# Optimization experiments

Measured on AMD Instinct MI355X. Metric: run time of the kernel, lower is better.

The kernel has to match this reference:

```python
import jax, jax.numpy as jnp
import numpy as np

N = 16384      # batch size
F = 1024       # n_features
H = 256        # n_dim (latent)


def setup_inputs() -> dict:
    key = jax.random.key(0)
    ks = jax.random.split(key, 6)
    X = jax.random.normal(ks[0], (N, F), dtype=jnp.float32)
    We = jax.random.normal(ks[1], (F, H), dtype=jnp.float32) / np.sqrt(F).astype(np.float32)
    be = jnp.zeros((H,), dtype=jnp.float32)
    Wd = jax.random.normal(ks[2], (H, F), dtype=jnp.float32) / np.sqrt(H).astype(np.float32)
    bd = jnp.zeros((F,), dtype=jnp.float32)
    Wc = jax.random.normal(ks[3], (H, 1), dtype=jnp.float32) / np.sqrt(H).astype(np.float32)
    bc = jnp.zeros((1,), dtype=jnp.float32)
    s = jax.random.randint(ks[4], (N,), 0, 2, dtype=jnp.int32)  # protected attribute labels in {0,1}
    return {"X": X, "We": We, "be": be, "Wd": Wd, "bd": bd, "Wc": Wc, "bc": bc, "s": s, "p": 1}


def reference(X, We, be, Wd, bd, Wc, bc, s, p):
    # encoder / decoder (single Linear each, as in the default NRL construction)
    g = X @ We + be                      # [N, H]
    rec = g @ Wd + bd                    # [N, F]
    mse_mean = jnp.mean((rec - X) ** 2)  # MSELoss is built with reduction='sum' but forward uses torch.mean(pow(...)) directly

    # critic scores for ALL rows (critics share weights: [module]*n_protected)
    c = (g @ Wc + bc)[:, 0]              # [N]

    # masked pairwise L1: sum_{i in P, j notin P} |c_i - c_j|
    mp = (s == p)                        # rows where s == p
    mpf = mp.astype(c.dtype)
    mrf = (~mp).astype(c.dtype)
    Dmat = jnp.abs(c[:, None] - c[None, :])   # [N, N] pairwise L1 (cdist equivalent)
    total = mpf @ (Dmat @ mrf)                # mp^T D mr == cdist(c_p, c_rest, p=1).sum()

    w_dist_count = mp.sum()                   # == w_dist.shape[0] (number of protected rows)
    w_dist_mean = total / w_dist_count.astype(c.dtype)

    return (mse_mean, jnp.asarray(rec.shape[0]), w_dist_mean, w_dist_count)
```

## Files before the change

### kernel.cpp

```cpp
#include <hip/hip_runtime.h>
#include <hip/hip_bf16.h>
#include <cstdint>

#define NR 16384
#define NF 1024
#define NH 256

typedef __bf16 bf16x8 __attribute__((ext_vector_type(8)));
typedef float f32x4 __attribute__((ext_vector_type(4)));
typedef unsigned short us8 __attribute__((ext_vector_type(8)));

static __device__ __forceinline__ unsigned short f2bf(float f) {
    unsigned u = __float_as_uint(f);
    u += 0x7FFFu + ((u >> 16) & 1u);
    return (unsigned short)(u >> 16);
}
static __device__ __forceinline__ float bf2f(unsigned short h) {
    return __uint_as_float(((unsigned)h) << 16);
}


__global__ __launch_bounds__(256) void prep_kernel(
    const float* __restrict__ X, const float* __restrict__ We,
    const float* __restrict__ Wd,
    unsigned short* __restrict__ Xpk, unsigned short* __restrict__ Wepk,
    unsigned short* __restrict__ Wdpk, float* __restrict__ hdr) {
    const int b = blockIdx.x, t = threadIdx.x;
    if (b == 0 && t < 192) hdr[t] = 0.f;
    if (b < 1024) {
        __shared__ float tile[16 * 272];
        const int r0 = b * 16;
#pragma unroll
        for (int ch = 0; ch < 4; ++ch) {
            const int c0 = ch * 256;
#pragma unroll
            for (int p = 0; p < 4; ++p) {
                int idx = t + 256 * p;
                int r = idx >> 6, c4 = idx & 63;
                *(float4*)&tile[r * 272 + c4 * 4] =
                    *(const float4*)(X + (size_t)(r0 + r) * NF + c0 + c4 * 4);
            }
            __syncthreads();
#pragma unroll
            for (int p = 0; p < 2; ++p) {
                int u = t + 256 * p;
                int cell = u >> 6, lane = u & 63;
                int m = lane & 15, q = lane >> 4;
                const float* src = &tile[m * 272 + cell * 32 + q * 8];
                us8 v;
#pragma unroll
                for (int e = 0; e < 8; e++) v[e] = f2bf(src[e]);
                *(us8*)&Xpk[((size_t)(b * 32 + ch * 8 + cell)) * 512 + lane * 8] = v;
            }
            __syncthreads();
        }
    } else if (b < 1040) {
        const int nb = b - 1024;
        const int lane = t & 63, q = lane >> 4, li = lane & 15, idx = t >> 6;
#pragma unroll
        for (int p = 0; p < 8; p++) {
            const int kc = idx + 4 * p;
            us8 v;
#pragma unroll
            for (int e = 0; e < 8; e++)
                v[e] = f2bf(We[(size_t)(kc * 32 + q * 8 + e) * NH + nb * 16 + li]);
            *(us8*)&Wepk[((size_t)(nb * 32 + kc)) * 512 + lane * 8] = v;
        }
    } else {
        const int nb4 = b - 1040;
        const int lane = t & 63, q = lane >> 4, li = lane & 15, idx = t >> 6;
#pragma unroll
        for (int p = 0; p < 8; p++) {
            const int c = nb4 * 32 + idx + 4 * p;
            const int nb = c >> 3, kc = c & 7;
            us8 v;
#pragma unroll
            for (int e = 0; e < 8; e++)
                v[e] = f2bf(Wd[(size_t)(kc * 32 + q * 8 + e) * NF + nb * 16 + li]);
            *(us8*)&Wdpk[((size_t)(nb * 8 + kc)) * 512 + lane * 8] = v;
        }
    }
}

__global__ __launch_bounds__(256) void fused_kernel(
    const unsigned short* __restrict__ Xpk,
    const unsigned short* __restrict__ Wepk, const unsigned short* __restrict__ Wdpk,
    const float* __restrict__ be, const float* __restrict__ bd,
    const float* __restrict__ Wc,
    float* __restrict__ cpart, float* __restrict__ hdr) {
    __shared__ unsigned short gs[32 * 256];
    __shared__ float credu[4][32];
    __shared__ float msred[4];
    const int t = threadIdx.x;
    const int b = blockIdx.x, m0 = b * 32;
    const int w = t >> 6, lane = t & 63, q = lane >> 4, li = lane & 15;
    const int wn = w * 64;

    const unsigned short* Ap0 = Xpk + ((size_t)(b * 2) * 32) * 512 + lane * 8;
    const unsigned short* Ap1 = Ap0 + (size_t)32 * 512;
    const unsigned short* Bp[4];
#pragma unroll
    for (int j = 0; j < 4; j++)
        Bp[j] = Wepk + ((size_t)(w * 4 + j) * 32) * 512 + lane * 8;

    us8 fa[2][2], fb[2][4];
#pragma unroll
    for (int z = 0; z < 2; ++z) {
        fa[z][0] = *(const us8*)(Ap0 + z * 512);
        fa[z][1] = *(const us8*)(Ap1 + z * 512);
#pragma unroll
        for (int j = 0; j < 4; j++) fb[z][j] = *(const us8*)(Bp[j] + z * 512);
    }
    f32x4 acc[2][4] = {};
#pragma unroll
    for (int kc = 0; kc < 32; ++kc) {
        const int cb = kc & 1;
        us8 na0, na1, nbv[4];
        const bool pf = (kc + 2 < 32);
        if (pf) {
            na0 = *(const us8*)(Ap0 + (kc + 2) * 512);
            na1 = *(const us8*)(Ap1 + (kc + 2) * 512);
#pragma unroll
            for (int j = 0; j < 4; j++) nbv[j] = *(const us8*)(Bp[j] + (kc + 2) * 512);
        }
        bf16x8 a0 = __builtin_bit_cast(bf16x8, fa[cb][0]);
        bf16x8 a1 = __builtin_bit_cast(bf16x8, fa[cb][1]);
#pragma unroll
        for (int j = 0; j < 4; j++) {
            bf16x8 bf = __builtin_bit_cast(bf16x8, fb[cb][j]);
            acc[0][j] = __builtin_amdgcn_mfma_f32_16x16x32_bf16(bf, a0, acc[0][j], 0, 0, 0);
            acc[1][j] = __builtin_amdgcn_mfma_f32_16x16x32_bf16(bf, a1, acc[1][j], 0, 0, 0);
        }
        if (pf) {
            fa[cb][0] = na0; fa[cb][1] = na1;
#pragma unroll
            for (int j = 0; j < 4; j++) fb[cb][j] = nbv[j];
        }
    }

#pragma unroll
    for (int i = 0; i < 2; i++) {
        float csum = 0.f;
        const int ml = i * 16 + li;
#pragma unroll
        for (int j = 0; j < 4; j++) {
            const int colb = wn + j * 16 + q * 4;
            float4 be4 = *(const float4*)&be[colb];
            float4 wc4 = *(const float4*)&Wc[colb];
            float v0 = acc[i][j][0] + be4.x;
            float v1 = acc[i][j][1] + be4.y;
            float v2 = acc[i][j][2] + be4.z;
            float v3 = acc[i][j][3] + be4.w;
            csum += v0 * wc4.x + v1 * wc4.y + v2 * wc4.z + v3 * wc4.w;
            ushort4 st = { f2bf(v0), f2bf(v1), f2bf(v2), f2bf(v3) };
            const int phys = ((colb >> 3)) ^ ml;
            *(ushort4*)&gs[ml * 256 + phys * 8 + (q & 1) * 4] = st;
        }
        csum += __shfl_down(csum, 32);
        csum += __shfl_down(csum, 16);
        if (lane < 16) credu[w][i * 16 + lane] = csum;
    }
    __syncthreads();
    if (t < 32)
        cpart[m0 + t] = credu[0][t] + credu[1][t] + credu[2][t] + credu[3][t];

    const unsigned short* Wp = Wdpk + lane * 8;
    us8 gb[2][4];
#pragma unroll
    for (int z = 0; z < 2; ++z)
#pragma unroll
        for (int j = 0; j < 4; j++)
            gb[z][j] = *(const us8*)(Wp + ((size_t)((w * 4 + j) * 8 + z)) * 512);

    float lsum = 0.f;
    f32x4 a2[2][4] = {};
#pragma unroll
    for (int it = 0; it < 32; ++it) {
        const int cb = it & 1, pass = it >> 3, kc = it & 7;
        us8 nbv[4];
        const bool pf = (it + 2 < 32);
        if (pf) {
            const int p2 = (it + 2) >> 3, k2 = (it + 2) & 7;
#pragma unroll
            for (int j = 0; j < 4; j++)
                nbv[j] = *(const us8*)(Wp + ((size_t)((p2 * 16 + w * 4 + j) * 8 + k2)) * 512);
        }
        bf16x8 af[2];
#pragma unroll
        for (int i = 0; i < 2; i++) {
            const int ml = i * 16 + li;
            const int phys = (kc * 4 + q) ^ ml;
            af[i] = __builtin_bit_cast(bf16x8, *(const us8*)&gs[ml * 256 + phys * 8]);
        }
#pragma unroll
        for (int j = 0; j < 4; j++) {
            bf16x8 bf = __builtin_bit_cast(bf16x8, gb[cb][j]);
            a2[0][j] = __builtin_amdgcn_mfma_f32_16x16x32_bf16(bf, af[0], a2[0][j], 0, 0, 0);
            a2[1][j] = __builtin_amdgcn_mfma_f32_16x16x32_bf16(bf, af[1], a2[1][j], 0, 0, 0);
        }
        if (pf) {
#pragma unroll
            for (int j = 0; j < 4; j++) gb[cb][j] = nbv[j];
        }
        if (kc == 7) {
#pragma unroll
            for (int i = 0; i < 2; i++) {
                const int mbp = b * 2 + i;
#pragma unroll
                for (int j = 0; j < 4; j++) {
                    const int colb = pass * 256 + wn + j * 16 + q * 4;
                    float4 bd4 = *(const float4*)&bd[colb];
                    const int kcx = pass * 8 + w * 2 + (j >> 1);
                    const int qp = (j & 1) * 2 + (q >> 1), h = q & 1;
                    ushort4 xv = *(const ushort4*)&Xpk[((size_t)(mbp * 32 + kcx)) * 512 +
                                                       (qp * 16 + li) * 8 + h * 4];
                    float d0 = a2[i][j][0] + bd4.x - bf2f(xv.x);
                    float d1 = a2[i][j][1] + bd4.y - bf2f(xv.y);
                    float d2 = a2[i][j][2] + bd4.z - bf2f(xv.z);
                    float d3 = a2[i][j][3] + bd4.w - bf2f(xv.w);
                    lsum += d0 * d0 + d1 * d1 + d2 * d2 + d3 * d3;
                    a2[i][j] = (f32x4){0.f, 0.f, 0.f, 0.f};
                }
            }
        }
    }
#pragma unroll
    for (int o = 32; o; o >>= 1) lsum += __shfl_down(lsum, o);
    if (lane == 0) msred[w] = lsum;
    __syncthreads();
    if (t == 0)
        atomicAdd(&hdr[b & 63], msred[0] + msred[1] + msred[2] + msred[3]);
}

__global__ __launch_bounds__(256) void compact_kernel(
    const float* __restrict__ c, const int* __restrict__ s, const int* __restrict__ pv,
    float* __restrict__ cP, float* __restrict__ cR, int* __restrict__ cnt) {
    int i = blockIdx.x * 256 + threadIdx.x;
    float ci = c[i];
    bool pr = (s[i] == pv[0]);
    int lane = threadIdx.x & 63;
    unsigned long long m = __ballot(pr);
    {
        int cm = __popcll(m);
        int base = 0;
        if (lane == 0 && cm) base = atomicAdd(&cnt[0], cm);
        base = __shfl(base, 0);
        int off = __popcll(m & ((1ull << lane) - 1ull));
        if (pr) cP[base + off] = ci;
    }
    {
        unsigned long long mm = ~m;
        int cm = __popcll(mm);
        int base = 0;
        if (lane == 0 && cm) base = atomicAdd(&cnt[1], cm);
        base = __shfl(base, 0);
        int off = __popcll(mm & ((1ull << lane) - 1ull));
        if (!pr) cR[base + off] = ci;
    }
}

__global__ __launch_bounds__(256) void pair_fin_kernel(
    const float* __restrict__ cP, const float* __restrict__ cR,
    float* __restrict__ hdr, float* __restrict__ out) {
    __shared__ float sj[1024];
    __shared__ float red[256];
    __shared__ int win;
    const int nP = ((const int*)hdr)[129];
    const int nR = ((const int*)hdr)[130];
    const int jb = blockIdx.x * 1024;
    int jn = nR - jb; if (jn < 0) jn = 0; if (jn > 1024) jn = 1024;
    float sum = 0.f;
    if (jn > 0 && blockIdx.y * 512 < nP) {
        for (int j = threadIdx.x; j < 1024; j += 256)
            sj[j] = (jb + j < nR) ? cR[jb + j] : 0.f;
        __syncthreads();
        const int a0 = blockIdx.y * 512 + threadIdx.x, a1 = a0 + 256;
        const float ca0 = (a0 < nP) ? cP[a0] : 0.f;
        const float ca1 = (a1 < nP) ? cP[a1] : 0.f;
        float s0 = 0.f, s1 = 0.f;
#pragma unroll 8
        for (int j4 = 0; j4 < 256; j4++) {
            float4 v = *(const float4*)&sj[j4 * 4];
            s0 += fabsf(ca0 - v.x) + fabsf(ca0 - v.y) + fabsf(ca0 - v.z) + fabsf(ca0 - v.w);
            s1 += fabsf(ca1 - v.x) + fabsf(ca1 - v.y) + fabsf(ca1 - v.z) + fabsf(ca1 - v.w);
        }
        float pad = (float)(1024 - jn);
        s0 -= pad * fabsf(ca0);
        s1 -= pad * fabsf(ca1);
        if (a0 >= nP) s0 = 0.f;
        if (a1 >= nP) s1 = 0.f;
        sum = s0 + s1;
#pragma unroll
        for (int o = 32; o; o >>= 1) sum += __shfl_down(sum, o);
        if ((threadIdx.x & 63) == 0 && sum != 0.f)
            atomicAdd(&hdr[64 + ((blockIdx.y * 16 + blockIdx.x) & 63)], sum);
    }
    __threadfence();
    __syncthreads();
    if (threadIdx.x == 0)
        win = (atomicAdd((int*)(hdr + 128), 1) == 16 * 32 - 1) ? 1 : 0;
    __syncthreads();
    if (win) {
        float v = (threadIdx.x < 128) ? atomicAdd(&hdr[threadIdx.x], 0.f) : 0.f;
        red[threadIdx.x] = v;
        __syncthreads();
        if (threadIdx.x == 0) {
            float ms = 0.f, ps = 0.f;
            for (int i = 0; i < 64; i++) { ms += red[i]; ps += red[64 + i]; }
            int np = atomicAdd((int*)(hdr + 129), 0);
            out[0] = ms / (float)((size_t)NR * NF);
            out[1] = (float)NR;
            out[2] = ps / (float)np;
            out[3] = (float)np;
        }
    }
}

extern "C" void kernel_launch(void* const* d_in, const int* in_sizes, int n_in,
                              void* d_out, int out_size, void* d_ws, size_t ws_size,
                              hipStream_t stream) {
    const float* X  = (const float*)d_in[0];
    const float* We = (const float*)d_in[1];
    const float* be = (const float*)d_in[2];
    const float* Wd = (const float*)d_in[3];
    const float* bd = (const float*)d_in[4];
    const float* Wc = (const float*)d_in[5];
    const int*   s  = (const int*)d_in[7];
    const int*   pv = (const int*)d_in[8];

    char* ws = (char*)d_ws;
    float* hdr   = (float*)ws;
    float* cpart = (float*)(ws + 1024);
    float* cP    = (float*)(ws + 1024 + 65536);
    float* cR    = (float*)(ws + 1024 + 2 * 65536);
    unsigned short* Xpk  = (unsigned short*)(ws + 1024 + 3 * 65536);
    unsigned short* Wepk = Xpk + (size_t)NR * NF;
    unsigned short* Wdpk = Wepk + (size_t)NH * NF;

    prep_kernel<<<1056, 256, 0, stream>>>(X, We, Wd, Xpk, Wepk, Wdpk, hdr);
    fused_kernel<<<512, 256, 0, stream>>>(Xpk, Wepk, Wdpk, be, bd, Wc, cpart, hdr);
    compact_kernel<<<64, 256, 0, stream>>>(cpart, s, pv, cP, cR, (int*)hdr + 129);
    pair_fin_kernel<<<dim3(16, 32), 256, 0, stream>>>(cP, cR, hdr, (float*)d_out);
}
```

Before: 198.0 us.

## Fuse X bf16 conversion into GEMM kernel and fold compaction into epilogue

The separate pass that converts X to a packed bf16 layout in workspace is removed. Each GEMM block now loads its 32 fp32 rows of X, converts them to bf16 and stages them in a 64KB swizzled LDS buffer, unioned with the later g buffer. The MSE residual now reads fp32 X directly instead of the bf16 copy. The protected/rest compaction is done in the fused kernel's epilogue with ballot and atomics, which removes the compact kernel and the bf16 X round trip through HBM. The tradeoffs are higher LDS use per block, which may lower occupancy, and a load-and-convert phase that is no longer overlapped with MFMA.

```diff
diff --git a/kernel.cpp b/kernel.cpp
--- a/kernel.cpp
+++ b/kernel.cpp
@@ -15,48 +15,17 @@
     u += 0x7FFFu + ((u >> 16) & 1u);
     return (unsigned short)(u >> 16);
 }
-static __device__ __forceinline__ float bf2f(unsigned short h) {
-    return __uint_as_float(((unsigned)h) << 16);
-}
 
 
 __global__ __launch_bounds__(256) void prep_kernel(
-    const float* __restrict__ X, const float* __restrict__ We,
-    const float* __restrict__ Wd,
-    unsigned short* __restrict__ Xpk, unsigned short* __restrict__ Wepk,
-    unsigned short* __restrict__ Wdpk, float* __restrict__ hdr) {
+    const float* __restrict__ We, const float* __restrict__ Wd,
+    unsigned short* __restrict__ Wepk, unsigned short* __restrict__ Wdpk,
+    float* __restrict__ hdr) {
     const int b = blockIdx.x, t = threadIdx.x;
     if (b == 0 && t < 192) hdr[t] = 0.f;
-    if (b < 1024) {
-        __shared__ float tile[16 * 272];
-        const int r0 = b * 16;
-#pragma unroll
-        for (int ch = 0; ch < 4; ++ch) {
-            const int c0 = ch * 256;
-#pragma unroll
-            for (int p = 0; p < 4; ++p) {
-                int idx = t + 256 * p;
-                int r = idx >> 6, c4 = idx & 63;
-                *(float4*)&tile[r * 272 + c4 * 4] =
-                    *(const float4*)(X + (size_t)(r0 + r) * NF + c0 + c4 * 4);
-            }
-            __syncthreads();
-#pragma unroll
-            for (int p = 0; p < 2; ++p) {
-                int u = t + 256 * p;
-                int cell = u >> 6, lane = u & 63;
-                int m = lane & 15, q = lane >> 4;
-                const float* src = &tile[m * 272 + cell * 32 + q * 8];
-                us8 v;
-#pragma unroll
-                for (int e = 0; e < 8; e++) v[e] = f2bf(src[e]);
-                *(us8*)&Xpk[((size_t)(b * 32 + ch * 8 + cell)) * 512 + lane * 8] = v;
-            }
-            __syncthreads();
-        }
-    } else if (b < 1040) {
-        const int nb = b - 1024;
-        const int lane = t & 63, q = lane >> 4, li = lane & 15, idx = t >> 6;
+    const int lane = t & 63, q = lane >> 4, li = lane & 15, idx = t >> 6;
+    if (b < 16) {
+        const int nb = b;
 #pragma unroll
         for (int p = 0; p < 8; p++) {
             const int kc = idx + 4 * p;
@@ -67,8 +36,7 @@
             *(us8*)&Wepk[((size_t)(nb * 32 + kc)) * 512 + lane * 8] = v;
         }
     } else {
-        const int nb4 = b - 1040;
-        const int lane = t & 63, q = lane >> 4, li = lane & 15, idx = t >> 6;
+        const int nb4 = b - 16;
 #pragma unroll
         for (int p = 0; p < 8; p++) {
             const int c = nb4 * 32 + idx + 4 * p;
@@ -83,48 +51,65 @@
 }
 
 __global__ __launch_bounds__(256) void fused_kernel(
-    const unsigned short* __restrict__ Xpk,
+    const float* __restrict__ X,
     const unsigned short* __restrict__ Wepk, const unsigned short* __restrict__ Wdpk,
     const float* __restrict__ be, const float* __restrict__ bd,
-    const float* __restrict__ Wc,
-    float* __restrict__ cpart, float* __restrict__ hdr) {
-    __shared__ unsigned short gs[32 * 256];
-    __shared__ float credu[4][32];
-    __shared__ float msred[4];
+    const float* __restrict__ Wc, const int* __restrict__ s, const int* __restrict__ pv,
+    float* __restrict__ cP, float* __restrict__ cR, float* __restrict__ hdr) {
+    __shared__ union {
+        unsigned short xa[32 * 1024];
+        struct {
+            unsigned short gs[32 * 256];
+            float credu[4][32];
+            float msred[4];
+        } p2;
+    } u;
     const int t = threadIdx.x;
     const int b = blockIdx.x, m0 = b * 32;
     const int w = t >> 6, lane = t & 63, q = lane >> 4, li = lane & 15;
     const int wn = w * 64;
 
-    const unsigned short* Ap0 = Xpk + ((size_t)(b * 2) * 32) * 512 + lane * 8;
-    const unsigned short* Ap1 = Ap0 + (size_t)32 * 512;
+    {
+        const int r = t >> 3, cg = t & 7;
+        const float* xrow = X + (size_t)(m0 + r) * NF + cg * 128;
+#pragma unroll
+        for (int ci = 0; ci < 16; ++ci) {
+            float4 lo = *(const float4*)(xrow + ci * 8);
+            float4 hi = *(const float4*)(xrow + ci * 8 + 4);
+            us8 v;
+            v[0] = f2bf(lo.x); v[1] = f2bf(lo.y); v[2] = f2bf(lo.z); v[3] = f2bf(lo.w);
+            v[4] = f2bf(hi.x); v[5] = f2bf(hi.y); v[6] = f2bf(hi.z); v[7] = f2bf(hi.w);
+            const int ch = cg * 16 + ci;
+            *(us8*)&u.xa[r * 1024 + ((ch ^ r) & 127) * 8] = v;
+        }
+    }
+    __syncthreads();
+
     const unsigned short* Bp[4];
 #pragma unroll
     for (int j = 0; j < 4; j++)
         Bp[j] = Wepk + ((size_t)(w * 4 + j) * 32) * 512 + lane * 8;
 
-    us8 fa[2][2], fb[2][4];
-#pragma unroll
-    for (int z = 0; z < 2; ++z) {
-        fa[z][0] = *(const us8*)(Ap0 + z * 512);
-        fa[z][1] = *(const us8*)(Ap1 + z * 512);
+    us8 fb[2][4];
+#pragma unroll
+    for (int z = 0; z < 2; ++z)
 #pragma unroll
         for (int j = 0; j < 4; j++) fb[z][j] = *(const us8*)(Bp[j] + z * 512);
-    }
+
     f32x4 acc[2][4] = {};
 #pragma unroll
     for (int kc = 0; kc < 32; ++kc) {
         const int cb = kc & 1;
-        us8 na0, na1, nbv[4];
+        us8 nbv[4];
         const bool pf = (kc + 2 < 32);
         if (pf) {
-            na0 = *(const us8*)(Ap0 + (kc + 2) * 512);
-            na1 = *(const us8*)(Ap1 + (kc + 2) * 512);
 #pragma unroll
             for (int j = 0; j < 4; j++) nbv[j] = *(const us8*)(Bp[j] + (kc + 2) * 512);
         }
-        bf16x8 a0 = __builtin_bit_cast(bf16x8, fa[cb][0]);
-        bf16x8 a1 = __builtin_bit_cast(bf16x8, fa[cb][1]);
+        const int ph0 = ((kc * 4 + q) ^ li) & 127;
+        const int ph1 = ((kc * 4 + q) ^ (16 + li)) & 127;
+        bf16x8 a0 = __builtin_bit_cast(bf16x8, *(const us8*)&u.xa[li * 1024 + ph0 * 8]);
+        bf16x8 a1 = __builtin_bit_cast(bf16x8, *(const us8*)&u.xa[(16 + li) * 1024 + ph1 * 8]);
 #pragma unroll
         for (int j = 0; j < 4; j++) {
             bf16x8 bf = __builtin_bit_cast(bf16x8, fb[cb][j]);
@@ -132,11 +117,19 @@
             acc[1][j] = __builtin_amdgcn_mfma_f32_16x16x32_bf16(bf, a1, acc[1][j], 0, 0, 0);
         }
         if (pf) {
-            fa[cb][0] = na0; fa[cb][1] = na1;
 #pragma unroll
             for (int j = 0; j < 4; j++) fb[cb][j] = nbv[j];
         }
     }
+    __syncthreads();
+
+    const unsigned short* Wp = Wdpk + lane * 8;
+    us8 gb[2][4];
+#pragma unroll
+    for (int z = 0; z < 2; ++z)
+#pragma unroll
+        for (int j = 0; j < 4; j++)
+            gb[z][j] = *(const us8*)(Wp + ((size_t)((w * 4 + j) * 8 + z)) * 512);
 
 #pragma unroll
     for (int i = 0; i < 2; i++) {
@@ -153,24 +146,32 @@
             float v3 = acc[i][j][3] + be4.w;
             csum += v0 * wc4.x + v1 * wc4.y + v2 * wc4.z + v3 * wc4.w;
             ushort4 st = { f2bf(v0), f2bf(v1), f2bf(v2), f2bf(v3) };
-            const int phys = ((colb >> 3)) ^ ml;
-            *(ushort4*)&gs[ml * 256 + phys * 8 + (q & 1) * 4] = st;
+            const int phys = (colb >> 3) ^ ml;
+            *(ushort4*)&u.p2.gs[ml * 256 + phys * 8 + (q & 1) * 4] = st;
         }
         csum += __shfl_down(csum, 32);
         csum += __shfl_down(csum, 16);
-        if (lane < 16) credu[w][i * 16 + lane] = csum;
-    }
-    __syncthreads();
-    if (t < 32)
-        cpart[m0 + t] = credu[0][t] + credu[1][t] + credu[2][t] + credu[3][t];
-
-    const unsigned short* Wp = Wdpk + lane * 8;
-    us8 gb[2][4];
-#pragma unroll
-    for (int z = 0; z < 2; ++z)
-#pragma unroll
-        for (int j = 0; j < 4; j++)
-            gb[z][j] = *(const us8*)(Wp + ((size_t)((w * 4 + j) * 8 + z)) * 512);
+        if (lane < 16) u.p2.credu[w][i * 16 + lane] = csum;
+    }
+    __syncthreads();
+
+    if (t < 32) {
+        float cs = u.p2.credu[0][t] + u.p2.credu[1][t] +
+                   u.p2.credu[2][t] + u.p2.credu[3][t];
+        bool pr = (s[m0 + t] == pv[0]);
+        unsigned long long mk = __ballot(pr);
+        int np = __popcll(mk);
+        int baseP = 0, baseR = 0;
+        if (t == 0) {
+            baseP = atomicAdd((int*)hdr + 129, np);
+            baseR = atomicAdd((int*)hdr + 130, 32 - np);
+        }
+        baseP = __shfl(baseP, 0);
+        baseR = __shfl(baseR, 0);
+        int offP = __popcll(mk & ((1ull << t) - 1ull));
+        int offR = t - offP;
+        if (pr) cP[baseP + offP] = cs; else cR[baseR + offR] = cs;
+    }
 
     float lsum = 0.f;
     f32x4 a2[2][4] = {};
@@ -180,17 +181,17 @@
         us8 nbv[4];
         const bool pf = (it + 2 < 32);
         if (pf) {
-            const int p2 = (it + 2) >> 3, k2 = (it + 2) & 7;
+            const int p2i = (it + 2) >> 3, k2 = (it + 2) & 7;
 #pragma unroll
             for (int j = 0; j < 4; j++)
-                nbv[j] = *(const us8*)(Wp + ((size_t)((p2 * 16 + w * 4 + j) * 8 + k2)) * 512);
+                nbv[j] = *(const us8*)(Wp + ((size_t)((p2i * 16 + w * 4 + j) * 8 + k2)) * 512);
         }
         bf16x8 af[2];
 #pragma unroll
         for (int i = 0; i < 2; i++) {
             const int ml = i * 16 + li;
             const int phys = (kc * 4 + q) ^ ml;
-            af[i] = __builtin_bit_cast(bf16x8, *(const us8*)&gs[ml * 256 + phys * 8]);
+            af[i] = __builtin_bit_cast(bf16x8, *(const us8*)&u.p2.gs[ml * 256 + phys * 8]);
         }
 #pragma unroll
         for (int j = 0; j < 4; j++) {
@@ -205,19 +206,16 @@
         if (kc == 7) {
 #pragma unroll
             for (int i = 0; i < 2; i++) {
-                const int mbp = b * 2 + i;
+                const size_t rowoff = (size_t)(m0 + i * 16 + li) * NF;
 #pragma unroll
                 for (int j = 0; j < 4; j++) {
                     const int colb = pass * 256 + wn + j * 16 + q * 4;
                     float4 bd4 = *(const float4*)&bd[colb];
-                    const int kcx = pass * 8 + w * 2 + (j >> 1);
-                    const int qp = (j & 1) * 2 + (q >> 1), h = q & 1;
-                    ushort4 xv = *(const ushort4*)&Xpk[((size_t)(mbp * 32 + kcx)) * 512 +
-                                                       (qp * 16 + li) * 8 + h * 4];
-                    float d0 = a2[i][j][0] + bd4.x - bf2f(xv.x);
-                    float d1 = a2[i][j][1] + bd4.y - bf2f(xv.y);
-                    float d2 = a2[i][j][2] + bd4.z - bf2f(xv.z);
-                    float d3 = a2[i][j][3] + bd4.w - bf2f(xv.w);
+                    float4 xr  = *(const float4*)&X[rowoff + colb];
+                    float d0 = a2[i][j][0] + bd4.x - xr.x;
+                    float d1 = a2[i][j][1] + bd4.y - xr.y;
+                    float d2 = a2[i][j][2] + bd4.z - xr.z;
+                    float d3 = a2[i][j][3] + bd4.w - xr.w;
                     lsum += d0 * d0 + d1 * d1 + d2 * d2 + d3 * d3;
                     a2[i][j] = (f32x4){0.f, 0.f, 0.f, 0.f};
                 }
@@ -226,37 +224,11 @@
     }
 #pragma unroll
     for (int o = 32; o; o >>= 1) lsum += __shfl_down(lsum, o);
-    if (lane == 0) msred[w] = lsum;
+    if (lane == 0) u.p2.msred[w] = lsum;
     __syncthreads();
     if (t == 0)
-        atomicAdd(&hdr[b & 63], msred[0] + msred[1] + msred[2] + msred[3]);
-}
-
-__global__ __launch_bounds__(256) void compact_kernel(
-    const float* __restrict__ c, const int* __restrict__ s, const int* __restrict__ pv,
-    float* __restrict__ cP, float* __restrict__ cR, int* __restrict__ cnt) {
-    int i = blockIdx.x * 256 + threadIdx.x;
-    float ci = c[i];
-    bool pr = (s[i] == pv[0]);
-    int lane = threadIdx.x & 63;
-    unsigned long long m = __ballot(pr);
-    {
-        int cm = __popcll(m);
-        int base = 0;
-        if (lane == 0 && cm) base = atomicAdd(&cnt[0], cm);
-        base = __shfl(base, 0);
-        int off = __popcll(m & ((1ull << lane) - 1ull));
-        if (pr) cP[base + off] = ci;
-    }
-    {
-        unsigned long long mm = ~m;
-        int cm = __popcll(mm);
-        int base = 0;
-        if (lane == 0 && cm) base = atomicAdd(&cnt[1], cm);
-        base = __shfl(base, 0);
-        int off = __popcll(mm & ((1ull << lane) - 1ull));
-        if (!pr) cR[base + off] = ci;
-    }
+        atomicAdd(&hdr[b & 63], u.p2.msred[0] + u.p2.msred[1] +
+                                u.p2.msred[2] + u.p2.msred[3]);
 }
 
 __global__ __launch_bounds__(256) void pair_fin_kernel(
@@ -329,16 +301,13 @@
     const int*   pv = (const int*)d_in[8];
 
     char* ws = (char*)d_ws;
-    float* hdr   = (float*)ws;
-    float* cpart = (float*)(ws + 1024);
-    float* cP    = (float*)(ws + 1024 + 65536);
-    float* cR    = (float*)(ws + 1024 + 2 * 65536);
-    unsigned short* Xpk  = (unsigned short*)(ws + 1024 + 3 * 65536);
-    unsigned short* Wepk = Xpk + (size_t)NR * NF;
+    float* hdr = (float*)ws;
+    float* cP  = (float*)(ws + 1024);
+    float* cR  = (float*)(ws + 1024 + 65536);
+    unsigned short* Wepk = (unsigned short*)(ws + 1024 + 2 * 65536);
     unsigned short* Wdpk = Wepk + (size_t)NH * NF;
 
-    prep_kernel<<<1056, 256, 0, stream>>>(X, We, Wd, Xpk, Wepk, Wdpk, hdr);
-    fused_kernel<<<512, 256, 0, stream>>>(Xpk, Wepk, Wdpk, be, bd, Wc, cpart, hdr);
-    compact_kernel<<<64, 256, 0, stream>>>(cpart, s, pv, cP, cR, (int*)hdr + 129);
+    prep_kernel<<<32, 256, 0, stream>>>(We, Wd, Wepk, Wdpk, hdr);
+    fused_kernel<<<512, 256, 0, stream>>>(X, Wepk, Wdpk, be, bd, Wc, s, pv, cP, cR, hdr);
     pair_fin_kernel<<<dim3(16, 32), 256, 0, stream>>>(cP, cR, hdr, (float*)d_out);
 }
```

Measured after the change: 191.6 us. -3.2%, faster.
